# Performance work log

Measured on AMD Instinct MI355X. Metric: run time of the kernel, lower is better.

Reference implementation:

```python
import jax, jax.numpy as jnp
import numpy as np

N_ATOM = 100000
N_BOND = 400000
N_GLOBAL = 5000
IN = 128
OUT = 128
HEADS = 2
NEG_SLOPE = 0.2
BN_EPS = 1e-5


def setup_inputs() -> dict:
    key = jax.random.key(0)
    ks = jax.random.split(key, 12)
    atom_feats = jax.random.normal(ks[0], (N_ATOM, IN), jnp.float32)
    bond_feats = jax.random.normal(ks[1], (N_BOND, IN), jnp.float32)
    global_feats = jax.random.normal(ks[2], (N_GLOBAL, IN), jnp.float32)
    W_atom = jax.random.normal(ks[3], (IN, OUT * HEADS), jnp.float32) * 0.05
    W_bond = jax.random.normal(ks[4], (IN, OUT * HEADS), jnp.float32) * 0.05
    W_global = jax.random.normal(ks[5], (IN, OUT * HEADS), jnp.float32) * 0.05
    attn_l = jax.random.normal(ks[6], (1, HEADS, OUT), jnp.float32) * 0.1
    attn_r = jax.random.normal(ks[7], (1, HEADS, OUT), jnp.float32) * 0.1
    bn_gamma = jnp.ones((OUT,), jnp.float32)
    bn_beta = jnp.zeros((OUT,), jnp.float32)
    bond_src = jax.random.randint(ks[8], (N_BOND,), 0, N_ATOM, jnp.int32)
    # ensure every atom appears as a bond destination at least once (DGL-like semantics)
    bond_dst = jnp.concatenate([
        jnp.arange(N_ATOM, dtype=jnp.int32),
        jax.random.randint(ks[9], (N_BOND - N_ATOM,), 0, N_ATOM, jnp.int32),
    ])
    g2a_src = jax.random.randint(ks[10], (N_ATOM,), 0, N_GLOBAL, jnp.int32)
    return dict(atom_feats=atom_feats, bond_feats=bond_feats, global_feats=global_feats,
                W_atom=W_atom, W_bond=W_bond, W_global=W_global,
                attn_l=attn_l, attn_r=attn_r, bn_gamma=bn_gamma, bn_beta=bn_beta,
                bond_src=bond_src, bond_dst=bond_dst, g2a_src=g2a_src)


def _fwd(atom_feats, bond_feats, global_feats, W_atom, W_bond, W_global,
         attn_l, attn_r, bn_gamma, bn_beta, bond_src, bond_dst, g2a_src):
    lrelu = lambda x: jax.nn.leaky_relu(x, NEG_SLOPE)
    # projections -> [*, H, D]
    h = (atom_feats @ W_atom).reshape(-1, HEADS, OUT)      # [N,H,D]
    e = (bond_feats @ W_bond).reshape(-1, HEADS, OUT)      # [E,H,D]
    u = (global_feats @ W_global).reshape(-1, HEADS, OUT)  # [G,H,D]
    er = (h * attn_r).sum(-1)    # [N,H]
    el_h = (h * attn_l).sum(-1)  # [N,H]
    el_e = (e * attn_l).sum(-1)  # [E,H]
    el_u = (u * attn_l).sum(-1)  # [G,H]
    er_dst = er[bond_dst]                      # [E,H]
    eh = lrelu(el_h[bond_src] + er_dst)        # bond: u_add_v
    ee = lrelu(el_e + er_dst)                  # bond: e_add_v
    eu = lrelu(el_u[g2a_src] + er)             # g2a: u_add_v (dst = arange(N))
    # numerically-stable edge softmax over both edge types per destination atom
    emax_b = jax.ops.segment_max(jnp.maximum(eh, ee), bond_dst, num_segments=N_ATOM)
    emax = jnp.maximum(emax_b, eu)             # [N,H]
    eh = jnp.exp(eh - emax[bond_dst])
    ee = jnp.exp(ee - emax[bond_dst])
    eu = jnp.exp(eu - emax)
    esum = jax.ops.segment_sum(eh + ee, bond_dst, num_segments=N_ATOM) + eu  # [N,H]
    esum_dst = esum[bond_dst]
    alpha_h = eh / esum_dst    # [E,H]
    alpha_e = ee / esum_dst
    alpha_u = eu / esum        # [N,H]
    msg = h[bond_src] * alpha_h[:, :, None] + e * alpha_e[:, :, None]  # [E,H,D]
    out = jax.ops.segment_sum(msg, bond_dst, num_segments=N_ATOM)
    out = out + u[g2a_src] * alpha_u[:, :, None]   # [N,H,D]
    hN = out.mean(axis=1)                           # mean over heads -> [N,D]
    # BatchNorm1d (training-mode batch stats, biased var)
    mean = hN.mean(axis=0)
    var = ((hN - mean) ** 2).mean(axis=0)
    hN = (hN - mean) * jax.lax.rsqrt(var + BN_EPS) * bn_gamma + bn_beta
    return jax.nn.relu(hN)


def reference(atom_feats, bond_feats, global_feats, W_atom, W_bond, W_global,
              attn_l, attn_r, bn_gamma, bn_beta, bond_src, bond_dst, g2a_src):
    return _fwd(atom_feats, bond_feats, global_feats, W_atom, W_bond, W_global,
                attn_l, attn_r, bn_gamma, bn_beta, bond_src, bond_dst, g2a_src)
```

## Files before the change

kernel.cpp:

```cpp
#include <hip/hip_runtime.h>
#include <hip/hip_bf16.h>

#define NA 100000
#define NB 400000
#define NG 5000
#define NEG 0.2f
#define KDIM 512
#define CAP 32
#define FG_BLKS 1563
#define KSC_BLKS 7891

typedef __attribute__((ext_vector_type(8))) short bf16x8;
typedef __attribute__((ext_vector_type(8))) unsigned short u16x8;
typedef __attribute__((ext_vector_type(4))) float f32x4;

__device__ __forceinline__ float lrelu(float x){ return x > 0.f ? x : NEG*x; }
__device__ __forceinline__ unsigned short f2bf(float f){
  unsigned u = __float_as_uint(f);
  u = (u + 0x7FFFu + ((u>>16)&1u)) >> 16;
  return (unsigned short)u;
}
__device__ __forceinline__ float bf2f(unsigned short s){
  return __uint_as_float(((unsigned)s) << 16);
}
__device__ __forceinline__ ushort2 pk2(float x, float y){
  __hip_bfloat162 t = __float22bfloat162_rn(make_float2(x, y));
  return *reinterpret_cast<ushort2*>(&t);
}

__global__ void kW(const float* __restrict__ Wa, const float* __restrict__ Wb,
                   const float* __restrict__ Wg, const float* __restrict__ glob,
                   const float* __restrict__ al, const float* __restrict__ ar,
                   unsigned short* wTa, unsigned short* wTb, unsigned short* wTu,
                   unsigned short* WcT, unsigned short* P){
  int blk = blockIdx.x;
  int tid = threadIdx.x;
  if (blk == 0){
    int k = tid >> 1, h = tid & 1;
    const float* wa = Wa + k*256 + h*128;
    const float* wb = Wb + k*256 + h*128;
    const float* wg = Wg + k*256 + h*128;
    const float* pl = al + h*128;
    const float* pr = ar + h*128;
    float sa=0.f, sra=0.f, se=0.f, su=0.f;
    for (int d=0; d<128; ++d){
      float L = pl[d], R = pr[d];
      sa  += wa[d]*L;  sra += wa[d]*R;
      se  += wb[d]*L;  su  += wg[d]*L;
    }
    wTa[h*128 + k]     = f2bf(sa);
    wTa[(2+h)*128 + k] = f2bf(sra);
    wTb[h*128 + k]     = f2bf(se);
    wTu[h*128 + k]     = f2bf(su);
    for (int idx = tid; idx < 14*128; idx += 256){
      int c = 2 + (idx >> 7), k2 = idx & 127;
      wTb[c*128 + k2] = 0;
      wTu[c*128 + k2] = 0;
      if (c >= 4) wTa[c*128 + k2] = 0;
    }
  } else if (blk <= 256){
    int idx = (blk-1)*256 + tid;
    int c = idx / KDIM, j = idx % KDIM;
    int part = j >> 7, k = j & 127;
    const float* W = (part < 2) ? Wa : Wb;
    int h = part & 1;
    WcT[(size_t)c*KDIM + j] = f2bf(0.5f * W[k*256 + h*128 + c]);
  } else {
    __shared__ float gl[8][128];
    int g0 = (blk-257)*8;
    #pragma unroll
    for (int r=0;r<4;++r){
      int idx = r*256+tid;
      gl[idx>>7][idx&127] = glob[(size_t)(g0 + (idx>>7))*128 + (idx&127)];
    }
    __syncthreads();
    float acc[8];
    #pragma unroll
    for (int g=0;g<8;++g) acc[g]=0.f;
    for (int k=0;k<128;++k){
      float wv = Wg[k*256 + tid];
      #pragma unroll
      for (int g=0;g<8;++g) acc[g] += gl[g][k]*wv;
    }
    #pragma unroll
    for (int g=0;g<8;++g)
      P[(size_t)(g0+g)*256 + tid] = f2bf(0.5f*acc[g]);
  }
}

__global__ __launch_bounds__(256) void kSC(
    const float* __restrict__ atom, const float* __restrict__ bond,
    const float* __restrict__ glob,
    const unsigned short* __restrict__ wTa, const unsigned short* __restrict__ wTb,
    const unsigned short* __restrict__ wTu,
    float* __restrict__ el_h, float* __restrict__ er,
    float* __restrict__ el_e, float* __restrict__ el_u,
    unsigned short* __restrict__ atomB, unsigned short* __restrict__ bondB){
  __shared__ unsigned short lds[4][16*128];
  const int wid = threadIdx.x >> 6;
  const int l = threadIdx.x & 63;
  const long rowbase = ((long)blockIdx.x*4 + wid) * 16;

  const float* feats; const unsigned short* wT; unsigned short* fb;
  long r0; long nrows; int type;
  if (rowbase < NA){            feats = atom; wT = wTa; fb = atomB; r0 = rowbase;          nrows = NA; type = 0; }
  else if (rowbase < NA+NB){    feats = bond; wT = wTb; fb = bondB; r0 = rowbase-NA;       nrows = NB; type = 1; }
  else {                        feats = glob; wT = wTu; fb = nullptr; r0 = rowbase-(NA+NB); nrows = NG; type = 2; }

  bf16x8 bfrag[4];
  #pragma unroll
  for (int kk=0;kk<4;++kk)
    bfrag[kk] = *reinterpret_cast<const bf16x8*>(wT + (size_t)(l&15)*128 + kk*32 + (l>>4)*8);

  unsigned short* wlds = lds[wid];
  const int j = l & 15;
  const int rl0 = l >> 4;
  #pragma unroll
  for (int i=0;i<4;++i){
    int rl = rl0 + i*4;
    long gr = r0 + rl;
    long grc = gr < nrows ? gr : (nrows-1);
    const float* src = feats + grc*128 + j*8;
    float4 x0 = *reinterpret_cast<const float4*>(src);
    float4 x1 = *reinterpret_cast<const float4*>(src+4);
    u16x8 w;
    ushort2 c0 = pk2(x0.x, x0.y), c1 = pk2(x0.z, x0.w);
    ushort2 c2 = pk2(x1.x, x1.y), c3 = pk2(x1.z, x1.w);
    w[0]=c0.x; w[1]=c0.y; w[2]=c1.x; w[3]=c1.y;
    w[4]=c2.x; w[5]=c2.y; w[6]=c3.x; w[7]=c3.y;
    *reinterpret_cast<u16x8*>(&wlds[rl*128 + ((j ^ (rl&7))*8)]) = w;
    if (fb && gr < nrows)
      *reinterpret_cast<u16x8*>(fb + grc*128 + j*8) = w;
  }
  __syncthreads();

  f32x4 acc = (f32x4){0.f,0.f,0.f,0.f};
  const int arow = l & 15;
  #pragma unroll
  for (int kk=0;kk<4;++kk){
    int ch = (kk*4 + (l>>4)) ^ (arow & 7);
    bf16x8 a = *reinterpret_cast<const bf16x8*>(&wlds[arow*128 + ch*8]);
    acc = __builtin_amdgcn_mfma_f32_16x16x32_bf16(a, bfrag[kk], acc, 0, 0, 0);
  }

  const int col = l & 15;
  if (col < 4 && (type == 0 || col < 2)){
    #pragma unroll
    for (int i=0;i<4;++i){
      long gr = r0 + (l>>4)*4 + i;
      if (gr < nrows){
        float v = acc[i];
        if (type == 0){
          if (col < 2) el_h[2*gr + col] = v;
          else         er[2*gr + col-2] = v;
        } else if (type == 1){
          el_e[2*gr + col] = v;
        } else {
          el_u[2*gr + col] = v;
        }
      }
    }
  }
}

__global__ void k4_edgeexp(const int* __restrict__ bsrc, const int* __restrict__ bdst,
                           const float* __restrict__ el_h, const float* __restrict__ er,
                           const float* __restrict__ el_e,
                           int2* __restrict__ slot_bs, float4* __restrict__ slot_e,
                           int* __restrict__ cursor, float* __restrict__ esum){
  int b = blockIdx.x*256 + threadIdx.x;
  if (b >= NB) return;
  int s = bsrc[b], d = bdst[b];
  float2 elh = *reinterpret_cast<const float2*>(&el_h[2*s]);
  float2 erd = *reinterpret_cast<const float2*>(&er[2*d]);
  float2 ele = *reinterpret_cast<const float2*>(&el_e[2*b]);
  float a0 = __expf(lrelu(elh.x + erd.x));
  float a1 = __expf(lrelu(elh.y + erd.y));
  float b0 = __expf(lrelu(ele.x + erd.x));
  float b1 = __expf(lrelu(ele.y + erd.y));
  int pos = atomicAdd(&cursor[d], 1);
  if (pos < CAP){
    slot_bs[(size_t)d*CAP + pos] = make_int2(b, s);
    slot_e [(size_t)d*CAP + pos] = make_float4(a0, a1, b0, b1);
  }
  atomicAdd(&esum[2*d],   a0 + b0);
  atomicAdd(&esum[2*d+1], a1 + b1);
}

__global__ __launch_bounds__(512, 2) void kFG(
    const unsigned short* __restrict__ atomB,
    const unsigned short* __restrict__ bondB,
    const int2* __restrict__ slot_bs, const float4* __restrict__ slot_e,
    const int* __restrict__ cursor, const float* __restrict__ esum,
    const float* __restrict__ el_u, const float* __restrict__ er,
    const int* __restrict__ g2a,
    const unsigned short* __restrict__ WcT,
    const unsigned short* __restrict__ P,
    float* __restrict__ out, float* __restrict__ colsum, float* __restrict__ colsq){
  __shared__ unsigned short XA[64*512];
  __shared__ float au_s[64][2];
  const int tid = threadIdx.x;
  const int l  = tid & 63;
  const int li = tid & 15;
  const int gid = tid >> 4;
  const int w = tid >> 6;
  const int wr = w >> 2, wc = w & 3;
  const int gb = l & 48;
  const int n0 = blockIdx.x * 64;

  for (int t=0; t<2; ++t){
    int ln = gid + t*32;
    int n = n0 + ln;
    float a0[8], a1[8], e0[8], e1[8];
    #pragma unroll
    for (int k2=0;k2<8;++k2){ a0[k2]=0.f; a1[k2]=0.f; e0[k2]=0.f; e1[k2]=0.f; }
    int cc = 0; float iv0=0.f, iv1=0.f, au0=0.f, au1=0.f;
    if (n < NA){
      cc = cursor[n]; cc = cc > CAP ? CAP : cc;
      int g = g2a[n];
      float2 elu = *reinterpret_cast<const float2*>(&el_u[2*g]);
      float2 ern = *reinterpret_cast<const float2*>(&er[2*n]);
      float u0 = __expf(lrelu(elu.x + ern.x));
      float u1 = __expf(lrelu(elu.y + ern.y));
      iv0 = 1.f/(esum[2*n]   + u0);
      iv1 = 1.f/(esum[2*n+1] + u1);
      au0 = u0*iv0; au1 = u1*iv1;
    }
    if (li == 0){ au_s[ln][0] = au0; au_s[ln][1] = au1; }

    int sA=0, bA=0, sB=0, bB=0;
    float4 eA = make_float4(0.f,0.f,0.f,0.f), eB = make_float4(0.f,0.f,0.f,0.f);
    if (li < cc){
      int2 bs = slot_bs[(size_t)n*CAP + li];
      bA = bs.x; sA = bs.y;
      eA = slot_e[(size_t)n*CAP + li];
    }
    if (li+16 < cc){
      int2 bs = slot_bs[(size_t)n*CAP + li+16];
      bB = bs.x; sB = bs.y;
      eB = slot_e[(size_t)n*CAP + li+16];
    }

    for (int w0=0; w0<cc; w0+=8){
      u16x8 ra[8], rb[8];
      #pragma unroll
      for (int jj=0;jj<8;++jj){
        int j = w0 + jj;
        if (j < cc){
          int sl = gb + (j & 15);
          int sj = (j < 16) ? __shfl(sA, sl) : __shfl(sB, sl);
          int bj = (j < 16) ? __shfl(bA, sl) : __shfl(bB, sl);
          ra[jj] = *reinterpret_cast<const u16x8*>(atomB + (size_t)sj*128 + li*8);
          rb[jj] = *reinterpret_cast<const u16x8*>(bondB + (size_t)bj*128 + li*8);
        }
      }
      #pragma unroll
      for (int jj=0;jj<8;++jj){
        int j = w0 + jj;
        if (j < cc){
          int sl = gb + (j & 15);
          float c0 = ((j<16) ? __shfl(eA.x, sl) : __shfl(eB.x, sl)) * iv0;
          float c1 = ((j<16) ? __shfl(eA.y, sl) : __shfl(eB.y, sl)) * iv1;
          float c2 = ((j<16) ? __shfl(eA.z, sl) : __shfl(eB.z, sl)) * iv0;
          float c3 = ((j<16) ? __shfl(eA.w, sl) : __shfl(eB.w, sl)) * iv1;
          #pragma unroll
          for (int k2=0;k2<8;++k2){
            float va = bf2f(ra[jj][k2]);
            float vb = bf2f(rb[jj][k2]);
            a0[k2] += c0*va; a1[k2] += c1*va;
            e0[k2] += c2*vb; e1[k2] += c3*vb;
          }
        }
      }
    }
    u16x8 o0, o1, o2, o3;
    #pragma unroll
    for (int k2=0;k2<8;++k2){
      o0[k2]=f2bf(a0[k2]); o1[k2]=f2bf(a1[k2]);
      o2[k2]=f2bf(e0[k2]); o3[k2]=f2bf(e1[k2]);
    }
    int xs = ln & 7;
    *reinterpret_cast<u16x8*>(&XA[ln*512 + (((0<<4)|li) ^ xs)*8]) = o0;
    *reinterpret_cast<u16x8*>(&XA[ln*512 + (((1<<4)|li) ^ xs)*8]) = o1;
    *reinterpret_cast<u16x8*>(&XA[ln*512 + (((2<<4)|li) ^ xs)*8]) = o2;
    *reinterpret_cast<u16x8*>(&XA[ln*512 + (((3<<4)|li) ^ xs)*8]) = o3;
  }
  __syncthreads();

  f32x4 acc[2][2];
  #pragma unroll
  for (int m=0;m<2;++m)
    #pragma unroll
    for (int nf=0;nf<2;++nf) acc[m][nf] = (f32x4){0.f,0.f,0.f,0.f};

  #pragma unroll
  for (int ks=0; ks<16; ++ks){
    bf16x8 av[2], bv[2];
    #pragma unroll
    for (int m=0;m<2;++m){
      int row = wr*32 + m*16 + (l & 15);
      int ch = (ks*4 + (l>>4)) ^ (row & 7);
      av[m] = *reinterpret_cast<const bf16x8*>(&XA[row*512 + ch*8]);
    }
    #pragma unroll
    for (int nf=0;nf<2;++nf){
      int col = wc*32 + nf*16 + (l & 15);
      bv[nf] = *reinterpret_cast<const bf16x8*>(
          WcT + (size_t)col*KDIM + ks*32 + (l>>4)*8);
    }
    #pragma unroll
    for (int m=0;m<2;++m)
      #pragma unroll
      for (int nf=0;nf<2;++nf)
        acc[m][nf] = __builtin_amdgcn_mfma_f32_16x16x32_bf16(av[m], bv[nf], acc[m][nf], 0, 0, 0);
  }

  float s[2] = {0.f,0.f};
  float q[2] = {0.f,0.f};
  #pragma unroll
  for (int m=0;m<2;++m){
    #pragma unroll
    for (int i=0;i<4;++i){
      int row_l = wr*32 + m*16 + (l>>4)*4 + i;
      size_t row = (size_t)n0 + row_l;
      if (row < NA){
        float aux = au_s[row_l][0], auy = au_s[row_l][1];
        int g = g2a[row];
        const unsigned short* Pg = P + (size_t)g*256;
        #pragma unroll
        for (int nf=0;nf<2;++nf){
          int col = wc*32 + nf*16 + (l&15);
          float v = acc[m][nf][i] + aux*bf2f(Pg[col]) + auy*bf2f(Pg[128+col]);
          out[row*128 + col] = v;
          s[nf] += v; q[nf] += v*v;
        }
      }
    }
  }
  #pragma unroll
  for (int nf=0;nf<2;++nf){
    int col = wc*32 + nf*16 + (l&15);
    float sv = s[nf], qv = q[nf];
    sv += __shfl_xor(sv, 16); sv += __shfl_xor(sv, 32);
    qv += __shfl_xor(qv, 16); qv += __shfl_xor(qv, 32);
    if (l < 16){
      atomicAdd(&colsum[col], sv);
      atomicAdd(&colsq[col],  qv);
    }
  }
}

__global__ __launch_bounds__(256) void k11_bnrelu(float* __restrict__ out,
                            const float* __restrict__ colsum, const float* __restrict__ colsq,
                            const float* __restrict__ gamma, const float* __restrict__ beta){
  __shared__ float sc[128], sh[128];
  int t = threadIdx.x;
  if (t < 128){
    float mean = colsum[t] / (float)NA;
    float var = fmaxf(colsq[t] / (float)NA - mean*mean, 0.f);
    float s = gamma[t] * rsqrtf(var + 1e-5f);
    sc[t] = s;
    sh[t] = beta[t] - mean*s;
  }
  __syncthreads();
  int i = blockIdx.x*256 + t;
  float4 v = reinterpret_cast<float4*>(out)[i];
  int c0 = (i*4) & 127;
  v.x = fmaxf(0.f, v.x*sc[c0]   + sh[c0]);
  v.y = fmaxf(0.f, v.y*sc[c0+1] + sh[c0+1]);
  v.z = fmaxf(0.f, v.z*sc[c0+2] + sh[c0+2]);
  v.w = fmaxf(0.f, v.w*sc[c0+3] + sh[c0+3]);
  reinterpret_cast<float4*>(out)[i] = v;
}

extern "C" void kernel_launch(void* const* d_in, const int* in_sizes, int n_in,
                              void* d_out, int out_size, void* d_ws, size_t ws_size,
                              hipStream_t stream) {
  const float* atom = (const float*)d_in[0];
  const float* bond = (const float*)d_in[1];
  const float* glob = (const float*)d_in[2];
  const float* Wa   = (const float*)d_in[3];
  const float* Wb   = (const float*)d_in[4];
  const float* Wg   = (const float*)d_in[5];
  const float* al   = (const float*)d_in[6];
  const float* ar   = (const float*)d_in[7];
  const float* gamma= (const float*)d_in[8];
  const float* beta = (const float*)d_in[9];
  const int* bsrc   = (const int*)d_in[10];
  const int* bdst   = (const int*)d_in[11];
  const int* g2a    = (const int*)d_in[12];
  float* out = (float*)d_out;

  char* base = (char*)d_ws;
  size_t off = 0;
  auto carve = [&](size_t bytes)->void*{
    void* p = base + off;
    off = (off + bytes + 255) & ~(size_t)255;
    return p;
  };
  unsigned short* wTa = (unsigned short*)carve((size_t)16*128*2);
  unsigned short* wTb = (unsigned short*)carve((size_t)16*128*2);
  unsigned short* wTu = (unsigned short*)carve((size_t)16*128*2);
  unsigned short* WcT = (unsigned short*)carve((size_t)128*KDIM*2);
  unsigned short* P   = (unsigned short*)carve((size_t)NG*256*2);
  float* el_h = (float*)carve((size_t)NA*2*4);
  float* er   = (float*)carve((size_t)NA*2*4);
  float* el_e = (float*)carve((size_t)NB*2*4);
  float* el_u = (float*)carve((size_t)NG*2*4);
  char* zr = (char*)carve((size_t)NA*2*4 + (size_t)NA*4 + 256*4);
  float* esum   = (float*)(zr);
  int*   cursor = (int*)(zr + (size_t)NA*2*4);
  float* colsum = (float*)(zr + (size_t)NA*2*4 + (size_t)NA*4);
  float* colsq  = colsum + 128;
  size_t zbytes = (size_t)NA*2*4 + (size_t)NA*4 + 256*4;
  int2*   slot_bs = (int2*)carve((size_t)NA*CAP*8);
  float4* slot_e  = (float4*)carve((size_t)NA*CAP*16);
  unsigned short* atomB = (unsigned short*)carve((size_t)NA*128*2);
  unsigned short* bondB = (unsigned short*)carve((size_t)NB*128*2);

  hipMemsetAsync(zr, 0, zbytes, stream);

  kW<<<882, 256, 0, stream>>>(Wa, Wb, Wg, glob, al, ar, wTa, wTb, wTu, WcT, P);

  kSC<<<KSC_BLKS, 256, 0, stream>>>(atom, bond, glob, wTa, wTb, wTu,
                                    el_h, er, el_e, el_u, atomB, bondB);

  k4_edgeexp<<<1563, 256, 0, stream>>>(bsrc, bdst, el_h, er, el_e,
                                       slot_bs, slot_e, cursor, esum);

  kFG<<<FG_BLKS, 512, 0, stream>>>(atomB, bondB, slot_bs, slot_e, cursor, esum,
                                   el_u, er, g2a, WcT, P, out, colsum, colsq);

  k11_bnrelu<<<12500, 256, 0, stream>>>(out, colsum, colsq, gamma, beta);
}
```

Before: 352.0 us.

## Software-pipeline gather loop in kFG, precompute per-node softmax terms, block-reduce BN stats

Adds a kPre kernel that computes per-atom inverse softmax sums, the global-attention coefficient and the clamped neighbor count, so kFG no longer does these dependent scalar loads and exps. kFG's neighbor gather loop becomes software-pipelined: it prefetches the next four atom/bond rows while consuming the current four, using clamped indices and zeroed weights in place of branches. Occupancy hint is raised to 4 blocks of 512 threads, and column-stat atomics are first reduced across waves in shared memory. The costs are one more launch, an extra per-node record array, some redundant loads past the neighbor count, and register pressure under the tighter launch bound.

```diff
diff --git a/kernel.cpp b/kernel.cpp
--- a/kernel.cpp
+++ b/kernel.cpp
@@ -187,18 +187,34 @@
   atomicAdd(&esum[2*d+1], a1 + b1);
 }
 
-__global__ __launch_bounds__(512, 2) void kFG(
+__global__ void kPre(const int* __restrict__ cursor, const float* __restrict__ esum,
+                     const float* __restrict__ el_u, const float* __restrict__ er,
+                     const int* __restrict__ g2a,
+                     float4* __restrict__ recF, int* __restrict__ recC){
+  int n = blockIdx.x*256 + threadIdx.x;
+  if (n >= NA) return;
+  int cc = cursor[n]; cc = cc > CAP ? CAP : cc;
+  int g = g2a[n];
+  float2 elu = *reinterpret_cast<const float2*>(&el_u[2*g]);
+  float2 ern = *reinterpret_cast<const float2*>(&er[2*n]);
+  float u0 = __expf(lrelu(elu.x + ern.x));
+  float u1 = __expf(lrelu(elu.y + ern.y));
+  float iv0 = 1.f/(esum[2*n]   + u0);
+  float iv1 = 1.f/(esum[2*n+1] + u1);
+  recF[n] = make_float4(iv0, iv1, u0*iv0, u1*iv1);
+  recC[n] = cc;
+}
+
+__global__ __launch_bounds__(512, 4) void kFG(
     const unsigned short* __restrict__ atomB,
     const unsigned short* __restrict__ bondB,
     const int2* __restrict__ slot_bs, const float4* __restrict__ slot_e,
-    const int* __restrict__ cursor, const float* __restrict__ esum,
-    const float* __restrict__ el_u, const float* __restrict__ er,
+    const float4* __restrict__ recF, const int* __restrict__ recC,
     const int* __restrict__ g2a,
     const unsigned short* __restrict__ WcT,
     const unsigned short* __restrict__ P,
     float* __restrict__ out, float* __restrict__ colsum, float* __restrict__ colsq){
   __shared__ unsigned short XA[64*512];
-  __shared__ float au_s[64][2];
   const int tid = threadIdx.x;
   const int l  = tid & 63;
   const int li = tid & 15;
@@ -208,28 +224,21 @@
   const int gb = l & 48;
   const int n0 = blockIdx.x * 64;
 
+  #pragma unroll
   for (int t=0; t<2; ++t){
     int ln = gid + t*32;
     int n = n0 + ln;
     float a0[8], a1[8], e0[8], e1[8];
     #pragma unroll
     for (int k2=0;k2<8;++k2){ a0[k2]=0.f; a1[k2]=0.f; e0[k2]=0.f; e1[k2]=0.f; }
-    int cc = 0; float iv0=0.f, iv1=0.f, au0=0.f, au1=0.f;
+    int cc = 0; float iv0=0.f, iv1=0.f;
     if (n < NA){
-      cc = cursor[n]; cc = cc > CAP ? CAP : cc;
-      int g = g2a[n];
-      float2 elu = *reinterpret_cast<const float2*>(&el_u[2*g]);
-      float2 ern = *reinterpret_cast<const float2*>(&er[2*n]);
-      float u0 = __expf(lrelu(elu.x + ern.x));
-      float u1 = __expf(lrelu(elu.y + ern.y));
-      iv0 = 1.f/(esum[2*n]   + u0);
-      iv1 = 1.f/(esum[2*n+1] + u1);
-      au0 = u0*iv0; au1 = u1*iv1;
-    }
-    if (li == 0){ au_s[ln][0] = au0; au_s[ln][1] = au1; }
-
-    int sA=0, bA=0, sB=0, bB=0;
-    float4 eA = make_float4(0.f,0.f,0.f,0.f), eB = make_float4(0.f,0.f,0.f,0.f);
+      cc = recC[n];
+      float4 rec = recF[n];
+      iv0 = rec.x; iv1 = rec.y;
+    }
+    int bA=0, sA=0, bB=0, sB=0;
+    float4 eA = make_float4(0.f,0.f,0.f,0.f), eB = eA;
     if (li < cc){
       int2 bs = slot_bs[(size_t)n*CAP + li];
       bA = bs.x; sA = bs.y;
@@ -240,38 +249,61 @@
       bB = bs.x; sB = bs.y;
       eB = slot_e[(size_t)n*CAP + li+16];
     }
-
-    for (int w0=0; w0<cc; w0+=8){
-      u16x8 ra[8], rb[8];
-      #pragma unroll
-      for (int jj=0;jj<8;++jj){
-        int j = w0 + jj;
-        if (j < cc){
-          int sl = gb + (j & 15);
-          int sj = (j < 16) ? __shfl(sA, sl) : __shfl(sB, sl);
-          int bj = (j < 16) ? __shfl(bA, sl) : __shfl(bB, sl);
-          ra[jj] = *reinterpret_cast<const u16x8*>(atomB + (size_t)sj*128 + li*8);
-          rb[jj] = *reinterpret_cast<const u16x8*>(bondB + (size_t)bj*128 + li*8);
-        }
+    if (cc > 0){
+      const int last = cc - 1;
+      #define IDXA(J) ({ int _jj = (J) <= last ? (J) : last; \
+                         int _sl = gb + (_jj & 15); \
+                         (_jj < 16) ? __shfl(sA, _sl) : __shfl(sB, _sl); })
+      #define IDXB(J) ({ int _jj = (J) <= last ? (J) : last; \
+                         int _sl = gb + (_jj & 15); \
+                         (_jj < 16) ? __shfl(bA, _sl) : __shfl(bB, _sl); })
+      u16x8 xa0 = *reinterpret_cast<const u16x8*>(atomB + (size_t)IDXA(0)*128 + li*8);
+      u16x8 xb0 = *reinterpret_cast<const u16x8*>(bondB + (size_t)IDXB(0)*128 + li*8);
+      u16x8 xa1 = *reinterpret_cast<const u16x8*>(atomB + (size_t)IDXA(1)*128 + li*8);
+      u16x8 xb1 = *reinterpret_cast<const u16x8*>(bondB + (size_t)IDXB(1)*128 + li*8);
+      u16x8 xa2 = *reinterpret_cast<const u16x8*>(atomB + (size_t)IDXA(2)*128 + li*8);
+      u16x8 xb2 = *reinterpret_cast<const u16x8*>(bondB + (size_t)IDXB(2)*128 + li*8);
+      u16x8 xa3 = *reinterpret_cast<const u16x8*>(atomB + (size_t)IDXA(3)*128 + li*8);
+      u16x8 xb3 = *reinterpret_cast<const u16x8*>(bondB + (size_t)IDXB(3)*128 + li*8);
+      for (int j0 = 0; j0 < cc; j0 += 4){
+        u16x8 ya0=xa0, ya1=xa1, ya2=xa2, ya3=xa3;
+        u16x8 yb0=xb0, yb1=xb1, yb2=xb2, yb3=xb3;
+        xa0 = *reinterpret_cast<const u16x8*>(atomB + (size_t)IDXA(j0+4)*128 + li*8);
+        xb0 = *reinterpret_cast<const u16x8*>(bondB + (size_t)IDXB(j0+4)*128 + li*8);
+        xa1 = *reinterpret_cast<const u16x8*>(atomB + (size_t)IDXA(j0+5)*128 + li*8);
+        xb1 = *reinterpret_cast<const u16x8*>(bondB + (size_t)IDXB(j0+5)*128 + li*8);
+        xa2 = *reinterpret_cast<const u16x8*>(atomB + (size_t)IDXA(j0+6)*128 + li*8);
+        xb2 = *reinterpret_cast<const u16x8*>(bondB + (size_t)IDXB(j0+6)*128 + li*8);
+        xa3 = *reinterpret_cast<const u16x8*>(atomB + (size_t)IDXA(j0+7)*128 + li*8);
+        xb3 = *reinterpret_cast<const u16x8*>(bondB + (size_t)IDXB(j0+7)*128 + li*8);
+        #define CONSUME(YA, YB, JJ) { \
+          int _j = j0 + (JJ); \
+          int _jc = _j <= last ? _j : last; \
+          int _sl = gb + (_jc & 15); \
+          float _wa0 = (_jc < 16) ? __shfl(eA.x, _sl) : __shfl(eB.x, _sl); \
+          float _wa1 = (_jc < 16) ? __shfl(eA.y, _sl) : __shfl(eB.y, _sl); \
+          float _wb0 = (_jc < 16) ? __shfl(eA.z, _sl) : __shfl(eB.z, _sl); \
+          float _wb1 = (_jc < 16) ? __shfl(eA.w, _sl) : __shfl(eB.w, _sl); \
+          bool _v = _j <= last; \
+          float _c0 = _v ? _wa0*iv0 : 0.f; \
+          float _c1 = _v ? _wa1*iv1 : 0.f; \
+          float _c2 = _v ? _wb0*iv0 : 0.f; \
+          float _c3 = _v ? _wb1*iv1 : 0.f; \
+          _Pragma("unroll") \
+          for (int k2=0;k2<8;++k2){ \
+            float _va = bf2f((YA)[k2]); \
+            float _vb = bf2f((YB)[k2]); \
+            a0[k2] += _c0*_va; a1[k2] += _c1*_va; \
+            e0[k2] += _c2*_vb; e1[k2] += _c3*_vb; \
+          } }
+        CONSUME(ya0, yb0, 0)
+        CONSUME(ya1, yb1, 1)
+        CONSUME(ya2, yb2, 2)
+        CONSUME(ya3, yb3, 3)
+        #undef CONSUME
       }
-      #pragma unroll
-      for (int jj=0;jj<8;++jj){
-        int j = w0 + jj;
-        if (j < cc){
-          int sl = gb + (j & 15);
-          float c0 = ((j<16) ? __shfl(eA.x, sl) : __shfl(eB.x, sl)) * iv0;
-          float c1 = ((j<16) ? __shfl(eA.y, sl) : __shfl(eB.y, sl)) * iv1;
-          float c2 = ((j<16) ? __shfl(eA.z, sl) : __shfl(eB.z, sl)) * iv0;
-          float c3 = ((j<16) ? __shfl(eA.w, sl) : __shfl(eB.w, sl)) * iv1;
-          #pragma unroll
-          for (int k2=0;k2<8;++k2){
-            float va = bf2f(ra[jj][k2]);
-            float vb = bf2f(rb[jj][k2]);
-            a0[k2] += c0*va; a1[k2] += c1*va;
-            e0[k2] += c2*vb; e1[k2] += c3*vb;
-          }
-        }
-      }
+      #undef IDXA
+      #undef IDXB
     }
     u16x8 o0, o1, o2, o3;
     #pragma unroll
@@ -280,10 +312,10 @@
       o2[k2]=f2bf(e0[k2]); o3[k2]=f2bf(e1[k2]);
     }
     int xs = ln & 7;
-    *reinterpret_cast<u16x8*>(&XA[ln*512 + (((0<<4)|li) ^ xs)*8]) = o0;
-    *reinterpret_cast<u16x8*>(&XA[ln*512 + (((1<<4)|li) ^ xs)*8]) = o1;
-    *reinterpret_cast<u16x8*>(&XA[ln*512 + (((2<<4)|li) ^ xs)*8]) = o2;
-    *reinterpret_cast<u16x8*>(&XA[ln*512 + (((3<<4)|li) ^ xs)*8]) = o3;
+    *reinterpret_cast<u16x8*>(&XA[ln*512 + ((li   ) ^ xs)*8]) = o0;
+    *reinterpret_cast<u16x8*>(&XA[ln*512 + ((16+li) ^ xs)*8]) = o1;
+    *reinterpret_cast<u16x8*>(&XA[ln*512 + ((32+li) ^ xs)*8]) = o2;
+    *reinterpret_cast<u16x8*>(&XA[ln*512 + ((48+li) ^ xs)*8]) = o3;
   }
   __syncthreads();
 
@@ -324,13 +356,13 @@
       int row_l = wr*32 + m*16 + (l>>4)*4 + i;
       size_t row = (size_t)n0 + row_l;
       if (row < NA){
-        float aux = au_s[row_l][0], auy = au_s[row_l][1];
+        float4 rec = recF[row];
         int g = g2a[row];
         const unsigned short* Pg = P + (size_t)g*256;
         #pragma unroll
         for (int nf=0;nf<2;++nf){
           int col = wc*32 + nf*16 + (l&15);
-          float v = acc[m][nf][i] + aux*bf2f(Pg[col]) + auy*bf2f(Pg[128+col]);
+          float v = acc[m][nf][i] + rec.z*bf2f(Pg[col]) + rec.w*bf2f(Pg[128+col]);
           out[row*128 + col] = v;
           s[nf] += v; q[nf] += v*v;
         }
@@ -339,14 +371,24 @@
   }
   #pragma unroll
   for (int nf=0;nf<2;++nf){
-    int col = wc*32 + nf*16 + (l&15);
-    float sv = s[nf], qv = q[nf];
-    sv += __shfl_xor(sv, 16); sv += __shfl_xor(sv, 32);
-    qv += __shfl_xor(qv, 16); qv += __shfl_xor(qv, 32);
-    if (l < 16){
-      atomicAdd(&colsum[col], sv);
-      atomicAdd(&colsq[col],  qv);
-    }
+    s[nf] += __shfl_xor(s[nf], 16); s[nf] += __shfl_xor(s[nf], 32);
+    q[nf] += __shfl_xor(q[nf], 16); q[nf] += __shfl_xor(q[nf], 32);
+  }
+  float* red = reinterpret_cast<float*>(XA);
+  __syncthreads();
+  if (l < 16){
+    #pragma unroll
+    for (int nf=0;nf<2;++nf){
+      red[      w*32 + nf*16 + li] = s[nf];
+      red[256 + w*32 + nf*16 + li] = q[nf];
+    }
+  }
+  __syncthreads();
+  if (tid < 256){
+    int h = tid >> 7, col = tid & 127;
+    int wcb = col >> 5, c5 = col & 31;
+    float v = red[h*256 + wcb*32 + c5] + red[h*256 + (4+wcb)*32 + c5];
+    atomicAdd((h ? colsq : colsum) + col, v);
   }
 }
 
@@ -407,6 +449,8 @@
   float* er   = (float*)carve((size_t)NA*2*4);
   float* el_e = (float*)carve((size_t)NB*2*4);
   float* el_u = (float*)carve((size_t)NG*2*4);
+  float4* recF = (float4*)carve((size_t)NA*16);
+  int*    recC = (int*)carve((size_t)NA*4);
   char* zr = (char*)carve((size_t)NA*2*4 + (size_t)NA*4 + 256*4);
   float* esum   = (float*)(zr);
   int*   cursor = (int*)(zr + (size_t)NA*2*4);
@@ -428,8 +472,10 @@
   k4_edgeexp<<<1563, 256, 0, stream>>>(bsrc, bdst, el_h, er, el_e,
                                        slot_bs, slot_e, cursor, esum);
 
-  kFG<<<FG_BLKS, 512, 0, stream>>>(atomB, bondB, slot_bs, slot_e, cursor, esum,
-                                   el_u, er, g2a, WcT, P, out, colsum, colsq);
+  kPre<<<391, 256, 0, stream>>>(cursor, esum, el_u, er, g2a, recF, recC);
+
+  kFG<<<FG_BLKS, 512, 0, stream>>>(atomB, bondB, slot_bs, slot_e, recF, recC,
+                                   g2a, WcT, P, out, colsum, colsq);
 
   k11_bnrelu<<<12500, 256, 0, stream>>>(out, colsum, colsq, gamma, beta);
 }
```

After: 324.6 us. 1.08x faster.
